# Kernel optimization log

Hardware: AMD Instinct MI355X
Metric: run time of the kernel (lower is better)

The kernel has to match this reference:

```python
import jax, jax.numpy as jnp
import numpy as np

TAU = 0.5    # __init__ tau
ALPHA = 1.0  # __init__ alpha
T_PARAM = 1.0  # self.T (non-trainable, ones)


def setup_inputs() -> dict:
    key = jax.random.key(0)
    k1, k2, k3 = jax.random.split(key, 3)
    B, C, H, W = 4, 64, 512, 512
    x = jax.random.normal(k1, (B, C, H, W), dtype=jnp.float32)
    # mirror torch init: xavier W, eig(W @ W.T) -> real eigenbasis Q, Qinv = inv(Q)
    Wm = jax.random.normal(k2, (C, C), dtype=jnp.float32) * float(np.sqrt(1.0 / C))
    M = Wm @ Wm.T  # symmetric PSD -> real eigendecomposition
    _, Q = jnp.linalg.eigh(M)
    Qinv = jnp.linalg.inv(Q)
    # trainable eigenvalue vector S (torch inits to ones; random positive here)
    S = jax.random.uniform(k3, (C,), dtype=jnp.float32, minval=0.1, maxval=1.1)
    return {"x": x, "S": S, "Q": Q, "Qinv": Qinv, "T": 5}


def reference(x, S, Q, Qinv, T):
    # Delta = (1/tau) * -1 * |S|**alpha   (passed to ExpDecay as its 'Delta')
    Delta = -(1.0 / TAU) * jnp.abs(S) ** ALPHA  # [C]
    # F.linear(x.permute(0,2,3,1), Q).permute(0,3,1,2)  ==  einsum over channel dim
    z = jnp.einsum('bchw,fc->bfhw', x, Q)
    # ExpDecay.step: diag(exp(T_total * Delta)) applied as elementwise channel scale
    t_total = T_PARAM * float(T)
    z2 = z * jnp.exp(t_total * Delta)[None, :, None, None]
    # F.linear(..., Qinv) back-projection
    return jnp.einsum('bchw,fc->bfhw', z2, Qinv)
```

## Files before the change

kernel.cpp:

```cpp
#include <hip/hip_runtime.h>
#include <hip/hip_bf16.h>
#include <math.h>


#define C_DIM 64
#define HW (512 * 512)

__global__ __launch_bounds__(256) void compute_M_kernel(
    const float* __restrict__ S, const float* __restrict__ Q,
    const float* __restrict__ Qinv, const int* __restrict__ Tp,
    float* __restrict__ M) {
    __shared__ float d[C_DIM];
    int tid = threadIdx.x;
    if (tid < C_DIM) {
        float t = (float)(*Tp);
        d[tid] = expf(-2.0f * t * fabsf(S[tid]));
    }
    __syncthreads();
    int gid = blockIdx.x * blockDim.x + tid;
    int f = gid >> 6;
    int k = gid & 63;
    float acc = 0.0f;
    #pragma unroll
    for (int c = 0; c < C_DIM; ++c) {
        acc = fmaf(Qinv[f * C_DIM + c] * d[c], Q[c * C_DIM + k], acc);
    }
    M[gid] = acc;
}

__global__ __launch_bounds__(256) void apply_M_kernel(
    const float* __restrict__ x, const float* __restrict__ M,
    float* __restrict__ out) {
    const int str2 = HW / 2;
    long long t = (long long)blockIdx.x * blockDim.x + threadIdx.x;
    long long base = t * 2;
    int b = (int)(base / HW);
    int s = (int)(base % HW);

    const float2* xp = (const float2*)(x + ((size_t)b * C_DIM) * HW + s);
    float2* op = (float2*)(out + ((size_t)b * C_DIM) * HW + s);

    float2 xv[C_DIM];
    #pragma unroll
    for (int c = 0; c < C_DIM; ++c) {
        xv[c] = xp[(size_t)c * str2];
    }

    #pragma unroll 1
    for (int f = 0; f < C_DIM; ++f) {
        float ax = 0.0f, ay = 0.0f;
        #pragma unroll
        for (int c = 0; c < C_DIM; ++c) {
            float m = M[f * C_DIM + c];
            ax = fmaf(m, xv[c].x, ax);
            ay = fmaf(m, xv[c].y, ay);
        }
        op[(size_t)f * str2] = make_float2(ax, ay);
    }
}

extern "C" void kernel_launch(void* const* d_in, const int* in_sizes, int n_in,
                              void* d_out, int out_size, void* d_ws, size_t ws_size,
                              hipStream_t stream) {
    const float* x    = (const float*)d_in[0];
    const float* S    = (const float*)d_in[1];
    const float* Q    = (const float*)d_in[2];
    const float* Qinv = (const float*)d_in[3];
    const int*   Tp   = (const int*)d_in[4];
    float* out = (float*)d_out;
    float* M = (float*)d_ws;

    compute_M_kernel<<<16, 256, 0, stream>>>(S, Q, Qinv, Tp, M);

    const int threads = 256;
    const int total_threads = (4 * HW) / 2;
    apply_M_kernel<<<total_threads / threads, threads, 0, stream>>>(x, M, out);
}
```

Before: 634.8 us.

## Restructure channel mix into chunked accumulation with prefetched input loads

New measurement: 524.0 us. 1.21x faster.

```diff
diff --git a/kernel.cpp b/kernel.cpp
--- a/kernel.cpp
+++ b/kernel.cpp
@@ -5,6 +5,7 @@
 
 #define C_DIM 64
 #define HW (512 * 512)
+#define CHUNK 16
 
 __global__ __launch_bounds__(256) void compute_M_kernel(
     const float* __restrict__ S, const float* __restrict__ Q,
@@ -28,35 +29,45 @@
     M[gid] = acc;
 }
 
-__global__ __launch_bounds__(256) void apply_M_kernel(
+__global__ __launch_bounds__(256, 4) void apply_M_kernel(
     const float* __restrict__ x, const float* __restrict__ M,
     float* __restrict__ out) {
-    const int str2 = HW / 2;
-    long long t = (long long)blockIdx.x * blockDim.x + threadIdx.x;
-    long long base = t * 2;
-    int b = (int)(base / HW);
-    int s = (int)(base % HW);
+    int t = blockIdx.x * 256 + threadIdx.x;
+    int b = t >> 18;
+    int s = t & (HW - 1);
 
-    const float2* xp = (const float2*)(x + ((size_t)b * C_DIM) * HW + s);
-    float2* op = (float2*)(out + ((size_t)b * C_DIM) * HW + s);
+    const float* xp = x + ((size_t)b * C_DIM) * HW + s;
+    float*       op = out + ((size_t)b * C_DIM) * HW + s;
 
-    float2 xv[C_DIM];
+    float acc[C_DIM];
     #pragma unroll
-    for (int c = 0; c < C_DIM; ++c) {
-        xv[c] = xp[(size_t)c * str2];
+    for (int f = 0; f < C_DIM; ++f) acc[f] = 0.0f;
+
+    float xv[CHUNK], xn[CHUNK];
+    #pragma unroll
+    for (int c = 0; c < CHUNK; ++c) xv[c] = xp[(size_t)c * HW];
+
+    #pragma unroll
+    for (int chunk = 0; chunk < C_DIM / CHUNK; ++chunk) {
+        if (chunk < C_DIM / CHUNK - 1) {
+            #pragma unroll
+            for (int c = 0; c < CHUNK; ++c)
+                xn[c] = xp[(size_t)((chunk + 1) * CHUNK + c) * HW];
+        }
+        #pragma unroll
+        for (int f = 0; f < C_DIM; ++f) {
+            float a = acc[f];
+            #pragma unroll
+            for (int c = 0; c < CHUNK; ++c)
+                a = fmaf(M[f * C_DIM + chunk * CHUNK + c], xv[c], a);
+            acc[f] = a;
+        }
+        #pragma unroll
+        for (int c = 0; c < CHUNK; ++c) xv[c] = xn[c];
     }
 
-    #pragma unroll 1
-    for (int f = 0; f < C_DIM; ++f) {
-        float ax = 0.0f, ay = 0.0f;
-        #pragma unroll
-        for (int c = 0; c < C_DIM; ++c) {
-            float m = M[f * C_DIM + c];
-            ax = fmaf(m, xv[c].x, ax);
-            ay = fmaf(m, xv[c].y, ay);
-        }
-        op[(size_t)f * str2] = make_float2(ax, ay);
-    }
+    #pragma unroll
+    for (int f = 0; f < C_DIM; ++f) op[(size_t)f * HW] = acc[f];
 }
 
 extern "C" void kernel_launch(void* const* d_in, const int* in_sizes, int n_in,
@@ -72,7 +83,5 @@
 
     compute_M_kernel<<<16, 256, 0, stream>>>(S, Q, Qinv, Tp, M);
 
-    const int threads = 256;
-    const int total_threads = (4 * HW) / 2;
-    apply_M_kernel<<<total_threads / threads, threads, 0, stream>>>(x, M, out);
+    apply_M_kernel<<<(4 * HW) / 256, 256, 0, stream>>>(x, M, out);
 }
```
